# Performance work log

Hardware: AMD Instinct MI355X
Metric: run time of the kernel (lower is better)

Reference implementation:

```python
import jax, jax.numpy as jnp
import numpy as np

DX = 64  # state dim
DY = 64  # observation dim
B = 64   # batch of independent series
T = 512  # time_extent


def setup_inputs() -> dict:
    key = jax.random.key(0)
    ks = jax.random.split(key, 9)
    Ix = jnp.eye(DX, dtype=jnp.float32)
    Iy = jnp.eye(DY, dtype=jnp.float32)
    observation = jax.random.normal(ks[0], (T + 1, B, DY), dtype=jnp.float32)
    prior_mean = 0.1 * jax.random.normal(ks[1], (DX,), dtype=jnp.float32)
    prior_chol = 0.3 * Ix + jnp.tril(0.02 * jax.random.normal(ks[2], (DX, DX), dtype=jnp.float32))
    dynamic_weight = 0.9 * Ix + 0.02 * jax.random.normal(ks[3], (DX, DX), dtype=jnp.float32)
    dynamic_bias = 0.01 * jax.random.normal(ks[4], (DX,), dtype=jnp.float32)
    dynamic_chol = 0.3 * Ix + jnp.tril(0.02 * jax.random.normal(ks[5], (DX, DX), dtype=jnp.float32))
    observation_weight = Iy + 0.05 * jax.random.normal(ks[6], (DY, DX), dtype=jnp.float32)
    observation_bias = 0.01 * jax.random.normal(ks[7], (DY,), dtype=jnp.float32)
    observation_chol = 0.3 * Iy + jnp.tril(0.02 * jax.random.normal(ks[8], (DY, DY), dtype=jnp.float32))
    return {
        "time_extent": T,
        "observation": observation,
        "prior_mean": prior_mean,
        "prior_chol": prior_chol,
        "dynamic_weight": dynamic_weight,
        "dynamic_bias": dynamic_bias,
        "dynamic_chol": dynamic_chol,
        "observation_weight": observation_weight,
        "observation_bias": observation_bias,
        "observation_chol": observation_chol,
    }


def reference(time_extent, observation, prior_mean, prior_chol, dynamic_weight,
              dynamic_bias, dynamic_chol, observation_weight, observation_bias,
              observation_chol):
    dtype = observation.dtype
    dx = prior_mean.shape[-1]
    dy = observation.shape[-1]
    b = observation.shape[1]
    half_log_2pi = 0.5 * jnp.log(jnp.asarray(2.0 * np.pi, dtype))

    P0 = prior_chol @ prior_chol.T            # (dx, dx) prior covariance
    Q = dynamic_chol @ dynamic_chol.T         # process noise
    R = observation_chol @ observation_chol.T # observation noise
    F = dynamic_weight
    H = observation_weight
    Ix = jnp.eye(dx, dtype=dtype)

    def log_density(mean, cov, y):
        # mean: (1,dy) or (b,dy); cov: (dy,dy); y: (b,dy)
        res = y - mean
        inv = jnp.linalg.inv(cov)
        pref = -dy * half_log_2pi - 0.5 * jnp.linalg.slogdet(cov)[1]
        return pref - 0.5 * jnp.einsum('bi,ij,bj->b', res, inv, res)

    def bayes_update(mean, P, y):
        # mean: (b,dx) or (1,dx); P: (dx,dx); y: (b,dy)
        CW = P @ H.T                               # (dx, dy)
        S_inv = jnp.linalg.inv(H @ CW + R)         # (dy, dy)
        WIW = H.T @ S_inv @ H                      # (dx, dx)
        post_P = P @ (Ix - WIW @ P)
        post_mean = mean @ (Ix - P @ WIW).T + (y - observation_bias) @ (CW @ S_inv).T
        return post_mean, post_P

    # t = 0: predictive of observation from the prior
    obs_mean0 = prior_mean[None, :] @ H.T + observation_bias  # (1, dy)
    obs_cov0 = H @ P0 @ H.T + R
    ll0 = log_density(obs_mean0, obs_cov0, observation[0])
    m0, P0_post = bayes_update(prior_mean[None, :], P0, observation[0])
    m0 = jnp.broadcast_to(m0, (b, dx))

    def step(carry, y):
        m, P = carry
        pm = m @ F.T + dynamic_bias                # predictive mean (b, dx)
        pP = F @ P @ F.T + Q                       # predictive cov (dx, dx)
        om = pm @ H.T + observation_bias           # obs predictive mean
        oC = H @ pP @ H.T + R
        ll = log_density(om, oC, y)
        nm, nP = bayes_update(pm, pP, y)
        return (nm, nP), (nm, nP, ll)

    (_, _), (ms, Ps, lls) = jax.lax.scan(step, (m0, P0_post), observation[1:])
    posterior_means = jnp.concatenate([m0[None], ms], axis=0)          # (T+1, b, dx)
    covs = jnp.concatenate([P0_post[None], Ps], axis=0)                # (T+1, dx, dx)
    posterior_covariances = jnp.broadcast_to(covs[:, None], (time_extent + 1, b, dx, dx))
    likelihood_factors = jnp.concatenate([ll0[None], lls], axis=0)     # (T+1, b)
    return posterior_means, posterior_covariances, likelihood_factors
```

## Files before the change

kernel.cpp:

```cpp
#include <hip/hip_runtime.h>
#include <math.h>


#define TID ((int)threadIdx.x)
#define LDA 68
#define MAT 4096
#define BSLOT 4096
#define NSLOT 513
#define HEAD 16
#define NTS 498
#define KMAX 5

#define WS_CSTAGE 0
#define WS_U      (NSLOT*MAT)
#define WS_EB     (WS_U + 9*MAT)
#define WS_CQ     (WS_EB + 4*MAT)
#define WS_CR     (WS_CQ + MAT)
#define WS_CHQ    (WS_CR + MAT)
#define WS_G      (WS_CHQ + MAT)
#define WS_KGT    (WS_G + MAT)
#define WS_HF     (WS_KGT + MAT)
#define WS_P0     (WS_HF + MAT)
#define WS_HP0    (WS_P0 + MAT)
#define WS_BA     (WS_HP0 + MAT)
#define WS_OBHDB  (WS_BA + 64)
#define WS_OM0    (WS_OBHDB + 64)
#define WS_HDB    (WS_OM0 + 64)
#define WS_SG     (WS_HDB + 64)
#define WS_B0     (WS_SG + MAT)
#define WS_B1     (WS_B0 + NSLOT*BSLOT)
#define WS_E0     (WS_B1 + NSLOT*BSLOT)
#define WS_E1     (WS_E0 + NSLOT*BSLOT)
#define WS_PP     (WS_E1 + NSLOT*BSLOT)
#define WS_SSI    (WS_PP + MAT)
#define WS_KST    (WS_SSI + MAT)
#define WS_BASS   (WS_KST + MAT)
#define WS_LDSS   (WS_BASS + 64)
#define WS_MK     (WS_LDSS + 64)

#define OUT_M 0
#define OUT_C 2101248
#define OUT_L 136581120

#define LLC (-58.81206612509905f)


__device__ __forceinline__ void tload(float* dst, const float* __restrict__ g) {
#pragma unroll
  for (int p = TID; p < 1024; p += 256) {
    int m = p >> 4, k4 = (p & 15) << 2;
    float4 v = *(const float4*)(g + m*64 + k4);
    dst[(k4+0)*LDA + m] = v.x;
    dst[(k4+1)*LDA + m] = v.y;
    dst[(k4+2)*LDA + m] = v.z;
    dst[(k4+3)*LDA + m] = v.w;
  }
}

__device__ __forceinline__ void tload_sub(float* dst, const float* __restrict__ g,
                                          const float* __restrict__ vec) {
#pragma unroll
  for (int p = TID; p < 1024; p += 256) {
    int m = p >> 4, k4 = (p & 15) << 2;
    float4 v = *(const float4*)(g + m*64 + k4);
    float4 s = *(const float4*)(vec + k4);
    dst[(k4+0)*LDA + m] = v.x - s.x;
    dst[(k4+1)*LDA + m] = v.y - s.y;
    dst[(k4+2)*LDA + m] = v.z - s.z;
    dst[(k4+3)*LDA + m] = v.w - s.w;
  }
}

__device__ __forceinline__ void pload(float* dst, const float* __restrict__ g) {
#pragma unroll
  for (int p = TID; p < 1024; p += 256) {
    int m = p >> 4, c4 = (p & 15) << 2;
    *(float4*)(dst + m*LDA + c4) = *(const float4*)(g + m*64 + c4);
  }
}

__device__ __forceinline__ void transcopy(float* dst, const float* src) {
#pragma unroll
  for (int p = TID; p < 1024; p += 256) {
    int m = p >> 4, k4 = (p & 15) << 2;
    float4 v = *(const float4*)(src + m*LDA + k4);
    dst[(k4+0)*LDA + m] = v.x;
    dst[(k4+1)*LDA + m] = v.y;
    dst[(k4+2)*LDA + m] = v.z;
    dst[(k4+3)*LDA + m] = v.w;
  }
}

__device__ __forceinline__ void gemm(const float* As, const float* Bs,
                                     float a[4][4], int tr, int tc) {
#pragma unroll
  for (int i = 0; i < 4; ++i)
#pragma unroll
    for (int j = 0; j < 4; ++j) a[i][j] = 0.f;
  const float* ap = As + (tr << 2);
  const float* bp = Bs + (tc << 2);
#pragma unroll 8
  for (int kk = 0; kk < 64; ++kk) {
    float4 av = *(const float4*)ap; ap += LDA;
    float4 bv = *(const float4*)bp; bp += LDA;
    a[0][0] = fmaf(av.x, bv.x, a[0][0]); a[0][1] = fmaf(av.x, bv.y, a[0][1]);
    a[0][2] = fmaf(av.x, bv.z, a[0][2]); a[0][3] = fmaf(av.x, bv.w, a[0][3]);
    a[1][0] = fmaf(av.y, bv.x, a[1][0]); a[1][1] = fmaf(av.y, bv.y, a[1][1]);
    a[1][2] = fmaf(av.y, bv.z, a[1][2]); a[1][3] = fmaf(av.y, bv.w, a[1][3]);
    a[2][0] = fmaf(av.z, bv.x, a[2][0]); a[2][1] = fmaf(av.z, bv.y, a[2][1]);
    a[2][2] = fmaf(av.z, bv.z, a[2][2]); a[2][3] = fmaf(av.z, bv.w, a[2][3]);
    a[3][0] = fmaf(av.w, bv.x, a[3][0]); a[3][1] = fmaf(av.w, bv.y, a[3][1]);
    a[3][2] = fmaf(av.w, bv.z, a[3][2]); a[3][3] = fmaf(av.w, bv.w, a[3][3]);
  }
}

__device__ __forceinline__ void add_g(float a[4][4], const float* __restrict__ g,
                                      int tr, int tc) {
#pragma unroll
  for (int i = 0; i < 4; ++i) {
    float4 v = *(const float4*)(g + (4*tr+i)*64 + 4*tc);
    a[i][0] += v.x; a[i][1] += v.y; a[i][2] += v.z; a[i][3] += v.w;
  }
}

__device__ __forceinline__ void rsub_g(float a[4][4], const float* __restrict__ g,
                                       int tr, int tc) {
#pragma unroll
  for (int i = 0; i < 4; ++i) {
    float4 v = *(const float4*)(g + (4*tr+i)*64 + 4*tc);
    a[i][0] = v.x - a[i][0]; a[i][1] = v.y - a[i][1];
    a[i][2] = v.z - a[i][2]; a[i][3] = v.w - a[i][3];
  }
}

__device__ __forceinline__ void addvec_g(float a[4][4], const float* __restrict__ v,
                                         int tc) {
  float4 s = *(const float4*)(v + 4*tc);
#pragma unroll
  for (int i = 0; i < 4; ++i) {
    a[i][0] += s.x; a[i][1] += s.y; a[i][2] += s.z; a[i][3] += s.w;
  }
}

__device__ __forceinline__ void addI(float a[4][4], int tr, int tc) {
  if (tr == tc) { a[0][0] += 1.f; a[1][1] += 1.f; a[2][2] += 1.f; a[3][3] += 1.f; }
}

__device__ __forceinline__ void gwrite(float* g, float a[4][4], int tr, int tc) {
#pragma unroll
  for (int i = 0; i < 4; ++i)
    *(float4*)(g + (4*tr+i)*64 + 4*tc) = make_float4(a[i][0], a[i][1], a[i][2], a[i][3]);
}

__device__ __forceinline__ void twrite_g(float* g, float a[4][4], int tr, int tc) {
#pragma unroll
  for (int i = 0; i < 4; ++i)
#pragma unroll
    for (int j = 0; j < 4; ++j)
      g[(4*tc+j)*64 + 4*tr+i] = a[i][j];
}

__device__ __forceinline__ void pstore(float* dst, float a[4][4], int tr, int tc) {
#pragma unroll
  for (int i = 0; i < 4; ++i)
    *(float4*)(dst + (4*tr+i)*LDA + 4*tc) = make_float4(a[i][0], a[i][1], a[i][2], a[i][3]);
}

__device__ __forceinline__ void tstore(float* dst, float a[4][4], int tr, int tc) {
#pragma unroll
  for (int i = 0; i < 4; ++i)
#pragma unroll
    for (int j = 0; j < 4; ++j)
      dst[(4*tc+j)*LDA + 4*tr+i] = a[i][j];
}

__device__ __forceinline__ void pwrite_g(float* g, const float* lds) {
#pragma unroll
  for (int p = TID; p < 1024; p += 256) {
    int m = p >> 4, c4 = (p & 15) << 2;
    *(float4*)(g + m*64 + c4) = *(const float4*)(lds + m*LDA + c4);
  }
}

__device__ float gj_inverse2(float* M, float* gjb, int wantLog) {
  const int i = TID >> 2, q = TID & 3;
  float r[16];
  {
    const float* base = M + i*LDA + 16*q;
    float4 v0 = *(const float4*)(base + 0);
    float4 v1 = *(const float4*)(base + 4);
    float4 v2 = *(const float4*)(base + 8);
    float4 v3 = *(const float4*)(base + 12);
    r[0]=v0.x; r[1]=v0.y; r[2]=v0.z; r[3]=v0.w;
    r[4]=v1.x; r[5]=v1.y; r[6]=v1.z; r[7]=v1.w;
    r[8]=v2.x; r[9]=v2.y; r[10]=v2.z; r[11]=v2.w;
    r[12]=v3.x; r[13]=v3.y; r[14]=v3.z; r[15]=v3.w;
  }
  float ld = 0.f;
  float* cb = gjb;
  float* rb = gjb + 128;
#pragma unroll 64
  for (int j = 0; j < 64; ++j) {
    float* cbp = cb + (j & 1) * 64;
    float* rbp = rb + (j & 1) * 64;
    if (q == (j >> 4)) cbp[i] = r[j & 15];
    if (i == j) {
      *(float4*)(rbp + 16*q + 0)  = make_float4(r[0], r[1], r[2], r[3]);
      *(float4*)(rbp + 16*q + 4)  = make_float4(r[4], r[5], r[6], r[7]);
      *(float4*)(rbp + 16*q + 8)  = make_float4(r[8], r[9], r[10], r[11]);
      *(float4*)(rbp + 16*q + 12) = make_float4(r[12], r[13], r[14], r[15]);
    }
    __syncthreads();
    float p = cbp[j];
    float rp = 1.0f / p;
    if (wantLog) ld += logf(p);
    float f = cbp[i];
    float mu = (i == j) ? (rp - 1.0f) : (0.0f - f * rp);
    float4 p0 = *(const float4*)(rbp + 16*q + 0);
    float4 p1 = *(const float4*)(rbp + 16*q + 4);
    float4 p2 = *(const float4*)(rbp + 16*q + 8);
    float4 p3 = *(const float4*)(rbp + 16*q + 12);
    r[0]  = fmaf(mu, p0.x, r[0]);  r[1]  = fmaf(mu, p0.y, r[1]);
    r[2]  = fmaf(mu, p0.z, r[2]);  r[3]  = fmaf(mu, p0.w, r[3]);
    r[4]  = fmaf(mu, p1.x, r[4]);  r[5]  = fmaf(mu, p1.y, r[5]);
    r[6]  = fmaf(mu, p1.z, r[6]);  r[7]  = fmaf(mu, p1.w, r[7]);
    r[8]  = fmaf(mu, p2.x, r[8]);  r[9]  = fmaf(mu, p2.y, r[9]);
    r[10] = fmaf(mu, p2.z, r[10]); r[11] = fmaf(mu, p2.w, r[11]);
    r[12] = fmaf(mu, p3.x, r[12]); r[13] = fmaf(mu, p3.y, r[13]);
    r[14] = fmaf(mu, p3.z, r[14]); r[15] = fmaf(mu, p3.w, r[15]);
    if (q == (j >> 4)) r[j & 15] = (i == j) ? rp : mu;
  }
  {
    float* base = M + i*LDA + 16*q;
    *(float4*)(base + 0)  = make_float4(r[0], r[1], r[2], r[3]);
    *(float4*)(base + 4)  = make_float4(r[4], r[5], r[6], r[7]);
    *(float4*)(base + 8)  = make_float4(r[8], r[9], r[10], r[11]);
    *(float4*)(base + 12) = make_float4(r[12], r[13], r[14], r[15]);
  }
  __syncthreads();
  return ld;
}

__device__ __forceinline__ int buf_parity(int s, int k) {
  if (s == 0) return 0;
  int li = 31 - __clz(s);
  int lu = li < (k - 1) ? li : (k - 1);
  return (lu + 1) & 1;
}

__device__ __forceinline__ float* bbuf(float* ws, int par) {
  return ws + (par ? WS_B1 : WS_B0);
}
__device__ __forceinline__ float* ebufp(float* ws, int par) {
  return ws + (par ? WS_E1 : WS_E0);
}

__device__ void prepA_body(int L, float* ws,
                           float* sA, float* sB, float* sT, float* sE,
                           float* gjb, int tr, int tc) {
  const float* AU = ws + WS_U + (size_t)(L % 3) * 3 * MAT;
  const float* CU = AU + MAT;
  const float* JU = AU + 2 * MAT;
  float* M2T = ws + WS_EB + (size_t)(L & 1) * 2 * MAT;
  float* EAo = M2T + MAT;
  float acc[4][4];

  pload(sA, CU); pload(sB, JU); __syncthreads();
  gemm(sA, sB, acc, tr, tc); addI(acc, tr, tc);
  __syncthreads(); pstore(sE, acc, tr, tc); __syncthreads();
  gj_inverse2(sE, gjb, 0);
  tload(sA, AU); __syncthreads();
  gemm(sA, sE, acc, tr, tc);
  twrite_g(M2T, acc, tr, tc);
  __syncthreads(); transcopy(sT, sE); pload(sB, AU); __syncthreads();
  gemm(sT, sB, acc, tr, tc);
  gwrite(EAo, acc, tr, tc);
}

__device__ void prepB1_body(int L, float* ws,
                            float* sA, float* sB, float* sT, float* sE,
                            float* gjb, int tr, int tc) {
  const float* AU = ws + WS_U + (size_t)(L % 3) * 3 * MAT;
  const float* CU = AU + MAT;
  const float* JU = AU + 2 * MAT;
  float* AUn = ws + WS_U + (size_t)((L + 1) % 3) * 3 * MAT;
  float* CUn = AUn + MAT;
  float acc[4][4];

  pload(sA, CU); pload(sB, JU); __syncthreads();
  gemm(sA, sB, acc, tr, tc); addI(acc, tr, tc);
  __syncthreads(); pstore(sE, acc, tr, tc); __syncthreads();
  gj_inverse2(sE, gjb, 0);
  tload(sB, AU); __syncthreads();
  gemm(sB, sE, acc, tr, tc);
  __syncthreads(); tstore(sT, acc, tr, tc); pload(sE, AU); __syncthreads();
  gemm(sT, sE, acc, tr, tc);
  gwrite(AUn, acc, tr, tc);
  gemm(sT, sA, acc, tr, tc);
  __syncthreads(); tstore(sE, acc, tr, tc); __syncthreads();
  gemm(sE, sB, acc, tr, tc);
  add_g(acc, CU, tr, tc); gwrite(CUn, acc, tr, tc);
}

__device__ void prepB2_body(int L, float* ws,
                            float* sA, float* sB, float* sT, float* sE,
                            float* gjb, int tr, int tc) {
  const float* AU = ws + WS_U + (size_t)(L % 3) * 3 * MAT;
  const float* CU = AU + MAT;
  const float* JU = AU + 2 * MAT;
  float* JUn = ws + WS_U + (size_t)((L + 1) % 3) * 3 * MAT + 2 * MAT;
  float acc[4][4];

  pload(sA, CU); pload(sB, JU); __syncthreads();
  gemm(sA, sB, acc, tr, tc); addI(acc, tr, tc);
  __syncthreads(); pstore(sE, acc, tr, tc); __syncthreads();
  gj_inverse2(sE, gjb, 0);
  gemm(sB, sE, acc, tr, tc);
  __syncthreads(); tstore(sT, acc, tr, tc); pload(sA, AU); __syncthreads();
  gemm(sT, sA, acc, tr, tc);
  __syncthreads(); pstore(sE, acc, tr, tc); __syncthreads();
  gemm(sA, sE, acc, tr, tc);
  add_g(acc, JU, tr, tc); gwrite(JUn, acc, tr, tc);
}

__device__ void bcast_part(const float* ws, float* out, int s, int part) {
  const float4* src = (const float4*)(ws + WS_CSTAGE + (size_t)s * MAT);
  float4 c0 = src[TID], c1 = src[TID+256], c2 = src[TID+512], c3 = src[TID+768];
  float4* dst = (float4*)(out + OUT_C + (size_t)s * 64 * MAT);
#pragma unroll
  for (int bb = part * 8; bb < part * 8 + 8; ++bb) {
    float4* d = dst + (size_t)bb * 1024;
    d[TID] = c0; d[TID+256] = c1; d[TID+512] = c2; d[TID+768] = c3;
  }
}

__device__ void bcast_ss_part(const float* ws, float* out, int s, int part) {
  const float4* src = (const float4*)(ws + WS_CSTAGE + (size_t)(HEAD-1) * MAT);
  float4 c0 = src[TID], c1 = src[TID+256], c2 = src[TID+512], c3 = src[TID+768];
  float4* dst = (float4*)(out + OUT_C + (size_t)s * 64 * MAT);
#pragma unroll
  for (int bb = part * 8; bb < part * 8 + 8; ++bb) {
    float4* d = dst + (size_t)bb * 1024;
    d[TID] = c0; d[TID+256] = c1; d[TID+512] = c2; d[TID+768] = c3;
  }
}

__device__ void ll_body(float* ws, float* out, const float* obs,
                        float* sA, float* sB, float* sT, float* sE,
                        float* gjb, int tr, int tc, int s) {
  int t = s + 1;
  const float* mp = out + OUT_M + (size_t)s * BSLOT;
  const float* Cp = ws + WS_CSTAGE + (size_t)s * MAT;
  float acc[4][4];

  tload(sA, ws + WS_HF); pload(sB, Cp); __syncthreads();
  gemm(sA, sB, acc, tr, tc);
  __syncthreads(); tstore(sT, acc, tr, tc); __syncthreads();
  gemm(sT, sA, acc, tr, tc);
  add_g(acc, ws + WS_SG, tr, tc);
  __syncthreads(); pstore(sE, acc, tr, tc); __syncthreads();
  float ldet = gj_inverse2(sE, gjb, 1);
  tload(sB, mp); __syncthreads();
  gemm(sB, sA, acc, tr, tc);
  addvec_g(acc, ws + WS_OBHDB, tc);
  const float* yt = obs + (size_t)t * BSLOT;
#pragma unroll
  for (int i2 = 0; i2 < 4; ++i2) {
    float4 v = *(const float4*)(yt + (4*tr+i2)*64 + 4*tc);
    acc[i2][0] = v.x - acc[i2][0]; acc[i2][1] = v.y - acc[i2][1];
    acc[i2][2] = v.z - acc[i2][2]; acc[i2][3] = v.w - acc[i2][3];
  }
  __syncthreads();
  pstore(sT, acc, tr, tc);
  tstore(sB, acc, tr, tc);
  __syncthreads();
  gemm(sB, sE, acc, tr, tc);
  __syncthreads(); pstore(sA, acc, tr, tc); __syncthreads();
  if (TID < 64) {
    float q = 0.f;
    for (int c = 0; c < 64; ++c) q = fmaf(sT[TID*LDA + c], sA[TID*LDA + c], q);
    out[OUT_L + (size_t)t * 64 + TID] = LLC - 0.5f * ldet - 0.5f * q;
  }
}

__device__ void ll_ss_body(float* ws, float* out, const float* obs,
                           float* sA, float* sB, float* sT, float* sE,
                           int tr, int tc, int t) {
  float acc[4][4];
  tload(sB, out + OUT_M + (size_t)(t - 1) * BSLOT);
  tload(sT, ws + WS_HF);
  pload(sE, ws + WS_SSI);
  __syncthreads();
  gemm(sB, sT, acc, tr, tc);
  addvec_g(acc, ws + WS_OBHDB, tc);
  const float* yt = obs + (size_t)t * BSLOT;
#pragma unroll
  for (int i2 = 0; i2 < 4; ++i2) {
    float4 v = *(const float4*)(yt + (4*tr+i2)*64 + 4*tc);
    acc[i2][0] = v.x - acc[i2][0]; acc[i2][1] = v.y - acc[i2][1];
    acc[i2][2] = v.z - acc[i2][2]; acc[i2][3] = v.w - acc[i2][3];
  }
  __syncthreads();
  pstore(sT, acc, tr, tc);
  tstore(sB, acc, tr, tc);
  __syncthreads();
  gemm(sB, sE, acc, tr, tc);
  __syncthreads(); pstore(sA, acc, tr, tc); __syncthreads();
  if (TID < 64) {
    float q = 0.f;
    for (int c = 0; c < 64; ++c) q = fmaf(sT[TID*LDA + c], sA[TID*LDA + c], q);
    out[OUT_L + (size_t)t * 64 + TID] = LLC - 0.5f * ws[WS_LDSS] - 0.5f * q;
  }
}

__global__ __launch_bounds__(256) void k_setup(
    float* ws, float* out, const float* obs, const float* pm, const float* pc,
    const float* F, const float* db, const float* dc, const float* H,
    const float* ob, const float* oc) {
  __shared__ __align__(16) float sA[64*LDA], sB[64*LDA], sT[64*LDA], sE[64*LDA];
  __shared__ __align__(16) float gjb[256];
  int tr = TID >> 4, tc = TID & 15;
  float acc[4][4];

  if (blockIdx.x == 0) {
    tload(sA, dc); __syncthreads();
    gemm(sA, sA, acc, tr, tc); gwrite(ws + WS_CQ, acc, tr, tc);
    __syncthreads();
    tload(sA, oc); __syncthreads();
    gemm(sA, sA, acc, tr, tc); gwrite(ws + WS_CR, acc, tr, tc);
    __syncthreads();
    tload(sA, H); pload(sB, ws + WS_CQ); __syncthreads();
    gemm(sA, sB, acc, tr, tc); gwrite(ws + WS_CHQ, acc, tr, tc);
    tstore(sT, acc, tr, tc);
    __syncthreads();
    gemm(sT, sA, acc, tr, tc); add_g(acc, ws + WS_CR, tr, tc);
    gwrite(ws + WS_SG, acc, tr, tc);
    __syncthreads(); pstore(sE, acc, tr, tc); __syncthreads();
    gj_inverse2(sE, gjb, 0);
    pload(sA, ws + WS_CHQ); __syncthreads();
    gemm(sA, sE, acc, tr, tc);
    twrite_g(ws + WS_KGT, acc, tr, tc);
    __syncthreads(); tstore(sT, acc, tr, tc); __syncthreads();
    tload(sA, H); pload(sB, F); __syncthreads();
    gemm(sA, sB, acc, tr, tc); gwrite(ws + WS_HF, acc, tr, tc);
    __syncthreads(); pstore(sB, acc, tr, tc); __syncthreads();
    gemm(sT, sB, acc, tr, tc); rsub_g(acc, F, tr, tc);
    gwrite(ws + WS_U + 0*MAT, acc, tr, tc);
    __syncthreads();
    pload(sB, ws + WS_CHQ); __syncthreads();
    gemm(sT, sB, acc, tr, tc); rsub_g(acc, ws + WS_CQ, tr, tc);
    gwrite(ws + WS_U + 1*MAT, acc, tr, tc);
    __syncthreads();
    pload(sB, ws + WS_HF); __syncthreads();
    gemm(sE, sB, acc, tr, tc);
    gwrite(ws + WS_G, acc, tr, tc);
    __syncthreads(); pstore(sT, acc, tr, tc); __syncthreads();
    gemm(sB, sT, acc, tr, tc);
    gwrite(ws + WS_U + 2*MAT, acc, tr, tc);
    __syncthreads();
    if (TID < 64) {
      float s = 0.f;
      for (int k = 0; k < 64; ++k) s = fmaf(H[TID*64 + k], db[k], s);
      ws[WS_HDB + TID] = s;
      ws[WS_OBHDB + TID] = s + ob[TID];
    }
    __syncthreads();
    if (TID < 64) {
      float s = 0.f;
      for (int k = 0; k < 64; ++k) s = fmaf(ws[WS_KGT + k*64 + TID], ws[WS_HDB + k], s);
      ws[WS_BA + TID] = db[TID] - s;
    }
  } else {
    float rt4[4][4];
    tload(sA, oc); __syncthreads();
    gemm(sA, sA, rt4, tr, tc);
    __syncthreads();
    tload(sA, pc); __syncthreads();
    gemm(sA, sA, acc, tr, tc);
    gwrite(ws + WS_P0, acc, tr, tc);
    __syncthreads(); pstore(sB, acc, tr, tc); __syncthreads();
    tload(sA, H); __syncthreads();
    gemm(sA, sB, acc, tr, tc);
    gwrite(ws + WS_HP0, acc, tr, tc);
    __syncthreads(); tstore(sT, acc, tr, tc); __syncthreads();
    gemm(sT, sA, acc, tr, tc);
#pragma unroll
    for (int i = 0; i < 4; ++i)
#pragma unroll
      for (int j = 0; j < 4; ++j) acc[i][j] += rt4[i][j];
    __syncthreads(); pstore(sE, acc, tr, tc); __syncthreads();
    float ldet = gj_inverse2(sE, gjb, 1);
    pload(sA, ws + WS_HP0); __syncthreads();
    gemm(sA, sE, acc, tr, tc);
    __syncthreads(); tstore(sT, acc, tr, tc); __syncthreads();
    pload(sB, ws + WS_HP0); __syncthreads();
    gemm(sT, sB, acc, tr, tc); rsub_g(acc, ws + WS_P0, tr, tc);
    gwrite(ws + WS_CSTAGE, acc, tr, tc);
    __syncthreads();
    if (TID < 64) {
      float s = 0.f;
      for (int k = 0; k < 64; ++k) s = fmaf(H[TID*64 + k], pm[k], s);
      ws[WS_OM0 + TID] = s + ob[TID];
    }
    __syncthreads();
    tload_sub(sA, obs, ws + WS_OM0); __syncthreads();
    gemm(sA, sT, acc, tr, tc); addvec_g(acc, pm, tc);
    gwrite(ws + WS_B0, acc, tr, tc);
    gwrite(out + OUT_M, acc, tr, tc);
    gemm(sA, sE, acc, tr, tc);
    __syncthreads(); pstore(sB, acc, tr, tc); __syncthreads();
    if (TID < 64) {
      float q = 0.f;
      for (int c = 0; c < 64; ++c) q = fmaf(sA[c*LDA + TID], sB[TID*LDA + c], q);
      out[OUT_L + TID] = LLC - 0.5f * ldet - 0.5f * q;
    }
    for (int idx = TID; idx < 4096; idx += 256) ws[WS_E0 + idx] = 0.f;
  }
}

__global__ __launch_bounds__(256) void k_init_head(
    float* ws, const float* obs, const float* ob) {
  __shared__ __align__(16) float sA[64*LDA], sB[64*LDA], sT[64*LDA], sE[64*LDA];
  __shared__ __align__(16) float gjb[256];
  int tr = TID >> 4, tc = TID & 15;
  int bid = blockIdx.x;
  if (bid >= HEAD - 1) {
    if (bid == HEAD - 1)      prepA_body(0, ws, sA, sB, sT, sE, gjb, tr, tc);
    else if (bid == HEAD)     prepB1_body(0, ws, sA, sB, sT, sE, gjb, tr, tc);
    else                      prepB2_body(0, ws, sA, sB, sT, sE, gjb, tr, tc);
    return;
  }
  int t = bid + 1;
  const float* yt = obs + (size_t)t * BSLOT;
  float acc[4][4];

  tload_sub(sA, yt, ob);
  pload(sB, ws + WS_KGT);
  __syncthreads();
  gemm(sA, sB, acc, tr, tc); addvec_g(acc, ws + WS_BA, tc);
  gwrite(ws + WS_B0 + (size_t)t * BSLOT, acc, tr, tc);
  __syncthreads();
  for (int idx = TID; idx < 4096; idx += 256) {
    int kk = idx >> 6, m = idx & 63;
    sA[kk*LDA + m] -= ws[WS_HDB + kk];
  }
  pload(sB, ws + WS_G);
  __syncthreads();
  gemm(sA, sB, acc, tr, tc);
  gwrite(ws + WS_E0 + (size_t)t * BSLOT, acc, tr, tc);
  (void)sT; (void)sE;
}

__global__ __launch_bounds__(256) void k_level_head(float* ws, float* out,
                                                    const float* obs, int k) {
  __shared__ __align__(16) float sA[64*LDA], sB[64*LDA], sT[64*LDA], sE[64*LDA];
  __shared__ __align__(16) float gjb[256];
  int tr = TID >> 4, tc = TID & 15;
  int bid = blockIdx.x;
  int nc = HEAD - (1 << k);

  if (bid < 3) {
    if (k <= 2) {
      if (bid == 0)      prepA_body(k + 1, ws, sA, sB, sT, sE, gjb, tr, tc);
      else if (bid == 1) prepB1_body(k + 1, ws, sA, sB, sT, sE, gjb, tr, tc);
      else               prepB2_body(k + 1, ws, sA, sB, sT, sE, gjb, tr, tc);
    }
    return;
  }
  if (bid >= 3 + nc) {
    int e = bid - (3 + nc);
    int ebase = k ? (1 << (k - 1)) : 0;
    bcast_part(ws, out, ebase + (e >> 3), e & 7);
    return;
  }

  int t = (1 << k) + bid - 3;
  int i = t - (1 << k);
  int pr = k & 1;
  int pw = (k + 1) & 1;
  int pl = buf_parity(i, k);
  const float* bi = bbuf(ws, pl) + (size_t)i * BSLOT;
  const float* ei = ebufp(ws, pl) + (size_t)i * BSLOT;
  const float* bj = bbuf(ws, pr) + (size_t)t * BSLOT;
  const float* ej = ebufp(ws, pr) + (size_t)t * BSLOT;
  float* bo = bbuf(ws, pw) + (size_t)t * BSLOT;
  float* eo = ebufp(ws, pw) + (size_t)t * BSLOT;
  const float* AU = ws + WS_U + (size_t)(k % 3) * 3 * MAT;
  const float* CU = AU + MAT;
  const float* JU = AU + 2 * MAT;
  const float* M2T = ws + WS_EB + (size_t)(k & 1) * 2 * MAT;
  const float* EAk = M2T + MAT;
  float acc[4][4];

  if (t >= (2 << k)) {
    tload(sA, ej); pload(sB, CU); __syncthreads();
    gemm(sA, sB, acc, tr, tc); add_g(acc, bi, tr, tc);
    tstore(sT, acc, tr, tc);
    __syncthreads();
    pload(sB, M2T); __syncthreads();
    gemm(sT, sB, acc, tr, tc); add_g(acc, bj, tr, tc);
    gwrite(bo, acc, tr, tc);
    __syncthreads();
    tload(sT, bi); pload(sB, JU); __syncthreads();
    gemm(sT, sB, acc, tr, tc);
#pragma unroll
    for (int i2 = 0; i2 < 4; ++i2)
#pragma unroll
      for (int j2 = 0; j2 < 4; ++j2) {
        int addr = (4*tc + j2)*LDA + 4*tr + i2;
        sA[addr] = sA[addr] - acc[i2][j2];
      }
    __syncthreads();
    pload(sB, EAk); __syncthreads();
    gemm(sA, sB, acc, tr, tc); add_g(acc, ei, tr, tc);
    gwrite(eo, acc, tr, tc);
  } else {
    const float* Ci = ws + WS_CSTAGE + (size_t)i * MAT;
    pload(sA, Ci); pload(sB, JU); __syncthreads();
    gemm(sA, sB, acc, tr, tc); addI(acc, tr, tc);
    __syncthreads(); pstore(sE, acc, tr, tc); __syncthreads();
    gj_inverse2(sE, gjb, 0);
    tload(sB, AU); __syncthreads();
    gemm(sB, sE, acc, tr, tc);
    __syncthreads(); tstore(sT, acc, tr, tc); __syncthreads();
    gemm(sT, sA, acc, tr, tc);
    __syncthreads(); tstore(sE, acc, tr, tc); __syncthreads();
    gemm(sE, sB, acc, tr, tc);
    add_g(acc, CU, tr, tc);
    gwrite(ws + WS_CSTAGE + (size_t)t * MAT, acc, tr, tc);
    __syncthreads();
    tload(sE, ej); __syncthreads();
    gemm(sE, sA, acc, tr, tc); add_g(acc, bi, tr, tc);
    __syncthreads(); tstore(sB, acc, tr, tc); __syncthreads();
    gemm(sB, sT, acc, tr, tc); add_g(acc, bj, tr, tc);
    gwrite(bo, acc, tr, tc);
    gwrite(out + OUT_M + (size_t)t * BSLOT, acc, tr, tc);
    (void)eo;
  }
}

__global__ __launch_bounds__(256) void k_ss(
    float* ws, float* out, const float* obs, const float* F, const float* H,
    const float* db) {
  __shared__ __align__(16) float sA[64*LDA], sB[64*LDA], sT[64*LDA], sE[64*LDA];
  __shared__ __align__(16) float gjb[256];
  int tr = TID >> 4, tc = TID & 15;
  int bid = blockIdx.x;

  if (bid == 65) {
    const float4* src = (const float4*)(out + OUT_M + (size_t)(HEAD-1) * BSLOT);
    float4* dst = (float4*)(ws + WS_B0);
#pragma unroll
    for (int q = 0; q < 4; ++q) dst[TID + 256*q] = src[TID + 256*q];
    return;
  }
  if (bid >= 1) {
    int b = bid - 1;
    bcast_part(ws, out, (HEAD/2) + (b >> 3), b & 7);
    return;
  }

  float acc[4][4];
  const float* Css = ws + WS_CSTAGE + (size_t)(HEAD-1) * MAT;
  tload(sA, F); pload(sB, Css); __syncthreads();
  gemm(sA, sB, acc, tr, tc);
  __syncthreads(); tstore(sT, acc, tr, tc); __syncthreads();
  gemm(sT, sA, acc, tr, tc); add_g(acc, ws + WS_CQ, tr, tc);
  gwrite(ws + WS_PP, acc, tr, tc);
  __syncthreads(); pstore(sB, acc, tr, tc); __syncthreads();
  tload(sA, H); __syncthreads();
  gemm(sA, sB, acc, tr, tc);
  __syncthreads(); tstore(sT, acc, tr, tc); __syncthreads();
  gemm(sT, sA, acc, tr, tc); add_g(acc, ws + WS_CR, tr, tc);
  __syncthreads(); pstore(sE, acc, tr, tc); __syncthreads();
  float ldet = gj_inverse2(sE, gjb, 1);
  pwrite_g(ws + WS_SSI, sE);
  if (TID == 0) ws[WS_LDSS] = ldet;
  pload(sB, ws + WS_PP); __syncthreads();
  gemm(sB, sA, acc, tr, tc);
  __syncthreads(); tstore(sT, acc, tr, tc); __syncthreads();
  gemm(sT, sE, acc, tr, tc);
  twrite_g(ws + WS_KST, acc, tr, tc);
  __syncthreads(); tstore(sT, acc, tr, tc); __syncthreads();
  pload(sB, H); __syncthreads();
  gemm(sT, sB, acc, tr, tc);
  __syncthreads(); tstore(sT, acc, tr, tc); __syncthreads();
  if (TID < 64) {
    float s = 0.f;
    for (int kk = 0; kk < 64; ++kk) s = fmaf(sT[kk*LDA + TID], db[kk], s);
    ws[WS_BASS + TID] = db[TID] - s;
  }
  pload(sB, F); __syncthreads();
  gemm(sT, sB, acc, tr, tc); rsub_g(acc, F, tr, tc);
  twrite_g(ws + WS_MK, acc, tr, tc);
}

__global__ __launch_bounds__(256) void k_tail_init(
    float* ws, float* out, const float* obs, const float* ob) {
  __shared__ __align__(16) float sA[64*LDA], sB[64*LDA], sT[64*LDA], sE[64*LDA];
  __shared__ __align__(16) float gjb[256];
  int tr = TID >> 4, tc = TID & 15;
  int bid = blockIdx.x;

  if (bid >= 513) {
    int b = bid - 513;
    bcast_ss_part(ws, out, HEAD + (b >> 3), b & 7);
    return;
  }
  if (bid >= 497) {
    ll_body(ws, out, obs, sA, sB, sT, sE, gjb, tr, tc, bid - 497);
    return;
  }
  int t = HEAD + bid;
  int i = bid + 1;
  float acc[4][4];

  tload_sub(sA, obs + (size_t)t * BSLOT, ob);
  pload(sB, ws + WS_KST);
  __syncthreads();
  gemm(sA, sB, acc, tr, tc); addvec_g(acc, ws + WS_BASS, tc);
  gwrite(ws + WS_B0 + (size_t)i * BSLOT, acc, tr, tc);
}

__global__ __launch_bounds__(256) void k_tail_level(float* ws, float* out,
                                                    const float* obs, int k) {
  __shared__ __align__(16) float sA[64*LDA], sB[64*LDA], sT[64*LDA], sE[64*LDA];
  int tr = TID >> 4, tc = TID & 15;
  int bid = blockIdx.x;
  int ntc = NTS - (1 << k);
  float acc[4][4];

  if (bid == 0) {
    if (k < KMAX) {
      const float* Mk = ws + WS_MK + (size_t)k * MAT;
      float* Mn = ws + WS_MK + (size_t)(k + 1) * MAT;
      tload(sA, Mk); pload(sB, Mk); __syncthreads();
      gemm(sA, sB, acc, tr, tc); gwrite(Mn, acc, tr, tc);
    }
    return;
  }
  if (bid < 1 + ntc) {
    int i = (1 << k) + bid - 1;
    int j = i - (1 << k);
    int pl = buf_parity(j, k);
    int pr = k & 1;
    int pw = (k + 1) & 1;
    const float* sj = bbuf(ws, pl) + (size_t)j * BSLOT;
    const float* si = bbuf(ws, pr) + (size_t)i * BSLOT;
    float* so = bbuf(ws, pw) + (size_t)i * BSLOT;
    tload(sA, sj); pload(sB, ws + WS_MK + (size_t)k * MAT); __syncthreads();
    gemm(sA, sB, acc, tr, tc); add_g(acc, si, tr, tc);
    gwrite(so, acc, tr, tc);
    if (k == KMAX || i < (2 << k))
      gwrite(out + OUT_M + (size_t)(HEAD - 1 + i) * BSLOT, acc, tr, tc);
    return;
  }
  int e = bid - (1 + ntc);
  int nll = k ? (1 << (k - 1)) : 1;
  if (e < nll) {
    int t = k ? (HEAD + (1 << (k - 1)) + e) : HEAD;
    ll_ss_body(ws, out, obs, sA, sB, sT, sE, tr, tc, t);
    return;
  }
  int b = e - nll;
  bcast_ss_part(ws, out, 101 + 58 * k + (b >> 3), b & 7);
}

__global__ __launch_bounds__(256) void k_tail_final(float* ws, float* out,
                                                    const float* obs) {
  __shared__ __align__(16) float sA[64*LDA], sB[64*LDA], sT[64*LDA], sE[64*LDA];
  int tr = TID >> 4, tc = TID & 15;
  int bid = blockIdx.x;
  if (bid < 465) {
    ll_ss_body(ws, out, obs, sA, sB, sT, sE, tr, tc, 48 + bid);
  } else {
    int b = bid - 465;
    bcast_ss_part(ws, out, 449 + (b >> 3), b & 7);
  }
}

extern "C" void kernel_launch(void* const* d_in, const int* in_sizes, int n_in,
                              void* d_out, int out_size, void* d_ws, size_t ws_size,
                              hipStream_t stream) {
  (void)in_sizes; (void)n_in; (void)out_size; (void)ws_size;
  const float* obs = (const float*)d_in[1];
  const float* pm  = (const float*)d_in[2];
  const float* pc  = (const float*)d_in[3];
  const float* F   = (const float*)d_in[4];
  const float* db  = (const float*)d_in[5];
  const float* dc  = (const float*)d_in[6];
  const float* H   = (const float*)d_in[7];
  const float* ob  = (const float*)d_in[8];
  const float* oc  = (const float*)d_in[9];
  float* out = (float*)d_out;
  float* ws  = (float*)d_ws;

  k_setup<<<dim3(2), dim3(256), 0, stream>>>(ws, out, obs, pm, pc, F, db, dc, H, ob, oc);
  k_init_head<<<dim3(HEAD + 2), dim3(256), 0, stream>>>(ws, obs, ob);
  for (int k = 0; k <= 3; ++k) {
    int nc = HEAD - (1 << k);
    int ec = k ? (1 << (k - 1)) : 1;
    k_level_head<<<dim3(3 + nc + 8 * ec), dim3(256), 0, stream>>>(ws, out, obs, k);
  }
  k_ss<<<dim3(66), dim3(256), 0, stream>>>(ws, out, obs, F, H, db);
  k_tail_init<<<dim3(497 + 16 + 680), dim3(256), 0, stream>>>(ws, out, obs, ob);
  for (int k = 0; k <= KMAX; ++k) {
    int ntc = NTS - (1 << k);
    int nll = k ? (1 << (k - 1)) : 1;
    k_tail_level<<<dim3(1 + ntc + nll + 464), dim3(256), 0, stream>>>(ws, out, obs, k);
  }
  k_tail_final<<<dim3(465 + 512), dim3(256), 0, stream>>>(ws, out, obs);
}
```

Baseline: 967.1 us.

## Replace six-level tail prefix scan with two-level radix-8 blocked scan

The steady-state tail mean recurrence was a Hillis-Steele scan over six kernel launches, each doing one 64x64 GEMM per slot. It becomes two levels of radix-8: the powers M^1..M^7 and (M^8)^1..(M^7) are precomputed, and each block accumulates up to seven GEMMs. This removes four launches and the global round trips between them, at the cost of more serial GEMMs and loads per block. Likelihood and broadcast work is redistributed across the remaining kernels to fill the grids.

```diff
diff --git a/kernel.cpp b/kernel.cpp
--- a/kernel.cpp
+++ b/kernel.cpp
@@ -9,7 +9,6 @@
 #define NSLOT 513
 #define HEAD 16
 #define NTS 498
-#define KMAX 5
 
 #define WS_CSTAGE 0
 #define WS_U      (NSLOT*MAT)
@@ -91,12 +90,8 @@
   }
 }
 
-__device__ __forceinline__ void gemm(const float* As, const float* Bs,
-                                     float a[4][4], int tr, int tc) {
-#pragma unroll
-  for (int i = 0; i < 4; ++i)
-#pragma unroll
-    for (int j = 0; j < 4; ++j) a[i][j] = 0.f;
+__device__ __forceinline__ void gemm_acc(const float* As, const float* Bs,
+                                         float a[4][4], int tr, int tc) {
   const float* ap = As + (tr << 2);
   const float* bp = Bs + (tc << 2);
 #pragma unroll 8
@@ -112,6 +107,15 @@
     a[3][0] = fmaf(av.w, bv.x, a[3][0]); a[3][1] = fmaf(av.w, bv.y, a[3][1]);
     a[3][2] = fmaf(av.w, bv.z, a[3][2]); a[3][3] = fmaf(av.w, bv.w, a[3][3]);
   }
+}
+
+__device__ __forceinline__ void gemm(const float* As, const float* Bs,
+                                     float a[4][4], int tr, int tc) {
+#pragma unroll
+  for (int i = 0; i < 4; ++i)
+#pragma unroll
+    for (int j = 0; j < 4; ++j) a[i][j] = 0.f;
+  gemm_acc(As, Bs, a, tr, tc);
 }
 
 __device__ __forceinline__ void add_g(float a[4][4], const float* __restrict__ g,
@@ -702,68 +706,146 @@
   int tr = TID >> 4, tc = TID & 15;
   int bid = blockIdx.x;
 
-  if (bid >= 513) {
-    int b = bid - 513;
+  if (bid < 16) {
+    ll_body(ws, out, obs, sA, sB, sT, sE, gjb, tr, tc, bid);
+    return;
+  }
+  if (bid == 16) {
+    float* MK0 = ws + WS_MK;
+    float acc[4][4], p4[4][4];
+    tload(sA, MK0); pload(sB, MK0); __syncthreads();
+    gemm(sA, sB, acc, tr, tc);
+    gwrite(MK0 + 1*MAT, acc, tr, tc);
+    pstore(sE, acc, tr, tc); tstore(sT, acc, tr, tc);
+    __syncthreads();
+    gemm(sA, sE, acc, tr, tc);
+    gwrite(MK0 + 2*MAT, acc, tr, tc);
+    __syncthreads();
+    tstore(sB, acc, tr, tc);
+    __syncthreads();
+    gemm(sT, sE, p4, tr, tc);
+    gwrite(MK0 + 3*MAT, p4, tr, tc);
+    __syncthreads();
+    pstore(sE, p4, tr, tc);
+    __syncthreads();
+    gemm(sA, sE, acc, tr, tc);
+    gwrite(MK0 + 4*MAT, acc, tr, tc);
+    __syncthreads();
+    tstore(sA, p4, tr, tc);
+    __syncthreads();
+    gemm(sT, sE, acc, tr, tc);
+    gwrite(MK0 + 5*MAT, acc, tr, tc);
+    gemm(sB, sE, acc, tr, tc);
+    gwrite(MK0 + 6*MAT, acc, tr, tc);
+    gemm(sA, sE, acc, tr, tc);
+    gwrite(MK0 + 7*MAT, acc, tr, tc);
+    return;
+  }
+  if (bid >= 514) {
+    int b = bid - 514;
     bcast_ss_part(ws, out, HEAD + (b >> 3), b & 7);
     return;
   }
-  if (bid >= 497) {
-    ll_body(ws, out, obs, sA, sB, sT, sE, gjb, tr, tc, bid - 497);
-    return;
-  }
-  int t = HEAD + bid;
-  int i = bid + 1;
-  float acc[4][4];
-
+  int i = bid - 16;
+  int t = 15 + i;
+  float acc[4][4];
   tload_sub(sA, obs + (size_t)t * BSLOT, ob);
   pload(sB, ws + WS_KST);
   __syncthreads();
   gemm(sA, sB, acc, tr, tc); addvec_g(acc, ws + WS_BASS, tc);
   gwrite(ws + WS_B0 + (size_t)i * BSLOT, acc, tr, tc);
-}
-
-__global__ __launch_bounds__(256) void k_tail_level(float* ws, float* out,
-                                                    const float* obs, int k) {
+  (void)sT; (void)sE;
+}
+
+__global__ __launch_bounds__(256) void k_tail_l0(float* ws, float* out) {
   __shared__ __align__(16) float sA[64*LDA], sB[64*LDA], sT[64*LDA], sE[64*LDA];
   int tr = TID >> 4, tc = TID & 15;
   int bid = blockIdx.x;
-  int ntc = NTS - (1 << k);
-  float acc[4][4];
 
   if (bid == 0) {
-    if (k < KMAX) {
-      const float* Mk = ws + WS_MK + (size_t)k * MAT;
-      float* Mn = ws + WS_MK + (size_t)(k + 1) * MAT;
-      tload(sA, Mk); pload(sB, Mk); __syncthreads();
-      gemm(sA, sB, acc, tr, tc); gwrite(Mn, acc, tr, tc);
-    }
-    return;
-  }
-  if (bid < 1 + ntc) {
-    int i = (1 << k) + bid - 1;
-    int j = i - (1 << k);
-    int pl = buf_parity(j, k);
-    int pr = k & 1;
-    int pw = (k + 1) & 1;
-    const float* sj = bbuf(ws, pl) + (size_t)j * BSLOT;
-    const float* si = bbuf(ws, pr) + (size_t)i * BSLOT;
-    float* so = bbuf(ws, pw) + (size_t)i * BSLOT;
-    tload(sA, sj); pload(sB, ws + WS_MK + (size_t)k * MAT); __syncthreads();
-    gemm(sA, sB, acc, tr, tc); add_g(acc, si, tr, tc);
-    gwrite(so, acc, tr, tc);
-    if (k == KMAX || i < (2 << k))
-      gwrite(out + OUT_M + (size_t)(HEAD - 1 + i) * BSLOT, acc, tr, tc);
-    return;
-  }
-  int e = bid - (1 + ntc);
-  int nll = k ? (1 << (k - 1)) : 1;
-  if (e < nll) {
-    int t = k ? (HEAD + (1 << (k - 1)) + e) : HEAD;
-    ll_ss_body(ws, out, obs, sA, sB, sT, sE, tr, tc, t);
-    return;
-  }
-  int b = e - nll;
-  bcast_ss_part(ws, out, 101 + 58 * k + (b >> 3), b & 7);
+    float* Q = ws + WS_MK + 7*MAT;
+    float acc[4][4], p4[4][4];
+    tload(sA, Q); pload(sB, Q); __syncthreads();
+    gemm(sA, sB, acc, tr, tc);
+    gwrite(Q + 1*MAT, acc, tr, tc);
+    pstore(sE, acc, tr, tc); tstore(sT, acc, tr, tc);
+    __syncthreads();
+    gemm(sA, sE, acc, tr, tc);
+    gwrite(Q + 2*MAT, acc, tr, tc);
+    __syncthreads();
+    tstore(sB, acc, tr, tc);
+    __syncthreads();
+    gemm(sT, sE, p4, tr, tc);
+    gwrite(Q + 3*MAT, p4, tr, tc);
+    __syncthreads();
+    pstore(sE, p4, tr, tc);
+    __syncthreads();
+    gemm(sA, sE, acc, tr, tc);
+    gwrite(Q + 4*MAT, acc, tr, tc);
+    gemm(sT, sE, acc, tr, tc);
+    gwrite(Q + 5*MAT, acc, tr, tc);
+    gemm(sB, sE, acc, tr, tc);
+    gwrite(Q + 6*MAT, acc, tr, tc);
+    return;
+  }
+  if (bid >= 498) {
+    int b = bid - 498;
+    bcast_ss_part(ws, out, 101 + (b >> 3), b & 7);
+    return;
+  }
+  int i = bid;
+  float acc[4][4];
+#pragma unroll
+  for (int a = 0; a < 4; ++a)
+#pragma unroll
+    for (int b2 = 0; b2 < 4; ++b2) acc[a][b2] = 0.f;
+  add_g(acc, ws + WS_B0 + (size_t)i * BSLOT, tr, tc);
+  int jm = i < 7 ? i : 7;
+  for (int j = 1; j <= jm; ++j) {
+    tload(sA, ws + WS_B0 + (size_t)(i - j) * BSLOT);
+    pload(sB, ws + WS_MK + (size_t)(j - 1) * MAT);
+    __syncthreads();
+    gemm_acc(sA, sB, acc, tr, tc);
+    __syncthreads();
+  }
+  gwrite(ws + WS_B1 + (size_t)i * BSLOT, acc, tr, tc);
+  if (i <= 7)
+    gwrite(out + OUT_M + (size_t)(15 + i) * BSLOT, acc, tr, tc);
+  (void)sT; (void)sE;
+}
+
+__global__ __launch_bounds__(256) void k_tail_l1(float* ws, float* out,
+                                                 const float* obs) {
+  __shared__ __align__(16) float sA[64*LDA], sB[64*LDA], sT[64*LDA], sE[64*LDA];
+  int tr = TID >> 4, tc = TID & 15;
+  int bid = blockIdx.x;
+
+  if (bid < 8) {
+    ll_ss_body(ws, out, obs, sA, sB, sT, sE, tr, tc, 16 + bid);
+    return;
+  }
+  if (bid >= 498) {
+    int b = bid - 498;
+    bcast_ss_part(ws, out, 251 + (b >> 3), b & 7);
+    return;
+  }
+  int i = bid;
+  float acc[4][4];
+#pragma unroll
+  for (int a = 0; a < 4; ++a)
+#pragma unroll
+    for (int b2 = 0; b2 < 4; ++b2) acc[a][b2] = 0.f;
+  add_g(acc, ws + WS_B1 + (size_t)i * BSLOT, tr, tc);
+  int rm = (i >> 3) < 7 ? (i >> 3) : 7;
+  for (int r = 1; r <= rm; ++r) {
+    tload(sA, ws + WS_B1 + (size_t)(i - 8 * r) * BSLOT);
+    pload(sB, ws + WS_MK + (size_t)(6 + r) * MAT);
+    __syncthreads();
+    gemm_acc(sA, sB, acc, tr, tc);
+    __syncthreads();
+  }
+  gwrite(out + OUT_M + (size_t)(15 + i) * BSLOT, acc, tr, tc);
+  (void)sT; (void)sE;
 }
 
 __global__ __launch_bounds__(256) void k_tail_final(float* ws, float* out,
@@ -771,11 +853,11 @@
   __shared__ __align__(16) float sA[64*LDA], sB[64*LDA], sT[64*LDA], sE[64*LDA];
   int tr = TID >> 4, tc = TID & 15;
   int bid = blockIdx.x;
-  if (bid < 465) {
-    ll_ss_body(ws, out, obs, sA, sB, sT, sE, tr, tc, 48 + bid);
+  if (bid < 489) {
+    ll_ss_body(ws, out, obs, sA, sB, sT, sE, tr, tc, 24 + bid);
   } else {
-    int b = bid - 465;
-    bcast_ss_part(ws, out, 449 + (b >> 3), b & 7);
+    int b = bid - 489;
+    bcast_ss_part(ws, out, 401 + (b >> 3), b & 7);
   }
 }
 
@@ -803,11 +885,8 @@
     k_level_head<<<dim3(3 + nc + 8 * ec), dim3(256), 0, stream>>>(ws, out, obs, k);
   }
   k_ss<<<dim3(66), dim3(256), 0, stream>>>(ws, out, obs, F, H, db);
-  k_tail_init<<<dim3(497 + 16 + 680), dim3(256), 0, stream>>>(ws, out, obs, ob);
-  for (int k = 0; k <= KMAX; ++k) {
-    int ntc = NTS - (1 << k);
-    int nll = k ? (1 << (k - 1)) : 1;
-    k_tail_level<<<dim3(1 + ntc + nll + 464), dim3(256), 0, stream>>>(ws, out, obs, k);
-  }
-  k_tail_final<<<dim3(465 + 512), dim3(256), 0, stream>>>(ws, out, obs);
-}
+  k_tail_init<<<dim3(16 + 1 + 497 + 680), dim3(256), 0, stream>>>(ws, out, obs, ob);
+  k_tail_l0<<<dim3(1 + 497 + 1200), dim3(256), 0, stream>>>(ws, out);
+  k_tail_l1<<<dim3(498 + 1200), dim3(256), 0, stream>>>(ws, out, obs);
+  k_tail_final<<<dim3(489 + 896), dim3(256), 0, stream>>>(ws, out, obs);
+}
```

After: 981.9 us. No clear change (+1.5%).
